# Kernel tuning notes

Hardware: AMD Instinct MI355X
Metric: run time of the kernel (lower is better)

Reference implementation:

```python
import jax, jax.numpy as jnp
import numpy as np

B, P, S, FX, FY, D, DFF = 8, 1, 2048, 16, 16, 512, 2048


def _ln(x, g, b, eps=1e-6):
    m = jnp.mean(x, axis=-1, keepdims=True)
    v = jnp.var(x, axis=-1, keepdims=True)
    return g * (x - m) / jnp.sqrt(v + eps) + b


def setup_inputs() -> dict:
    key = jax.random.key(0)
    ks = jax.random.split(key, 16)
    sc = 0.02
    inp = {
        'inputs': jax.random.normal(ks[0], (B, P, S, FX), dtype=jnp.float32),
        'targets': jax.random.normal(ks[1], (B, P, S, FY), dtype=jnp.float32),
        # input projection Dense(d_model)
        'Wp': jax.random.normal(ks[2], (FX, D), dtype=jnp.float32) * sc,
        'bp': jnp.zeros((D,), jnp.float32),
        # attention projections wq/wk/wv/dense (all Dense(d_model))
        'Wq': jax.random.normal(ks[3], (D, D), dtype=jnp.float32) * sc,
        'bq': jnp.zeros((D,), jnp.float32),
        'Wk': jax.random.normal(ks[4], (D, D), dtype=jnp.float32) * sc,
        'bk': jnp.zeros((D,), jnp.float32),
        'Wv': jax.random.normal(ks[5], (D, D), dtype=jnp.float32) * sc,
        'bv': jnp.zeros((D,), jnp.float32),
        'Wo': jax.random.normal(ks[6], (D, D), dtype=jnp.float32) * sc,
        'bo': jnp.zeros((D,), jnp.float32),
        # layernorm 1 / 2
        'g1': jnp.ones((D,), jnp.float32),
        'beta1': jnp.zeros((D,), jnp.float32),
        'g2': jnp.ones((D,), jnp.float32),
        'beta2': jnp.zeros((D,), jnp.float32),
        # pointwise FFN Dense(dff, relu) -> Dense(d_model)
        'Wf1': jax.random.normal(ks[7], (D, DFF), dtype=jnp.float32) * sc,
        'bf1': jnp.zeros((DFF,), jnp.float32),
        'Wf2': jax.random.normal(ks[8], (DFF, D), dtype=jnp.float32) * sc,
        'bf2': jnp.zeros((D,), jnp.float32),
        # final output layer Dense(output_size)
        'Wfin': jax.random.normal(ks[9], (D, FY), dtype=jnp.float32) * sc,
        'bfin': jnp.zeros((FY,), jnp.float32),
    }
    return inp


def reference(inputs, targets, Wp, bp, Wq, bq, Wk, bk, Wv, bv, Wo, bo,
              g1, beta1, g2, beta2, Wf1, bf1, Wf2, bf2, Wfin, bfin):
    d = jnp.float32(Wp.shape[1])
    # projection_layer_ts then *sqrt(d_model)
    x = (inputs @ Wp + bp) * jnp.sqrt(d)                      # (B,P,S,D)
    q = x @ Wq + bq
    k = x @ Wk + bk
    v = x @ Wv + bv
    # with noise=False and no resampling, the per-step SMC recurrence equals
    # causal self-attention (at step t, K/V hold rows <= t, rest are zero-masked)
    logits = jnp.einsum('bpqd,bpkd->bpqk', q, k) / jnp.sqrt(d)  # (B,P,S,S)
    Sdim = x.shape[2]
    causal = jnp.tril(jnp.ones((Sdim, Sdim), dtype=bool))
    logits = jnp.where(causal, logits, jnp.float32(-1e9))
    attn = jax.nn.softmax(logits, axis=-1)                    # attention weights per step
    z = jnp.einsum('bpqk,bpkd->bpqd', attn, v)
    z = z @ Wo + bo
    # full_model: LN(z+x) -> FFN -> LN(ffn+out)
    out = _ln(z + x, g1, beta1)
    ff = jax.nn.relu(out @ Wf1 + bf1) @ Wf2 + bf2
    r = _ln(ff + out, g2, beta2)                              # R trajectory (B,P,S,D)
    pred = r @ Wfin + bfin                                    # (B,P,S,F_y)
    # no resampling (noise=False): R_resampl == R, pred_resampl == pred
    return (pred, pred, k, v, r, attn)
```

## Files before the change

### kernel.cpp

```cpp
#include <hip/hip_runtime.h>
#include <hip/hip_bf16.h>
#include <stdint.h>

#define BB 8
#define SS 2048
#define TT (BB*SS)
#define DD 512
#define DFFX 2048

static __device__ const float SQRTD  = 22.627416997969522f;
static __device__ const float INVSQD = 0.04419417382415922f;

typedef __attribute__((ext_vector_type(4))) float  f32x4_t;
typedef __attribute__((ext_vector_type(8))) __bf16 bf16x8_t;
typedef __attribute__((ext_vector_type(4))) __bf16 bf16x4_t;

static __device__ __forceinline__ bf16x8_t mk_frag(bf16x4_t lo, bf16x4_t hi) {
  return __builtin_shufflevector(lo, hi, 0, 1, 2, 3, 4, 5, 6, 7);
}

typedef __attribute__((address_space(1))) const unsigned int g_u32;
typedef __attribute__((address_space(3))) unsigned int lds_u32;
static __device__ __forceinline__ void gld16(const void* g, void* l) {
  __builtin_amdgcn_global_load_lds((g_u32*)g, (lds_u32*)l, 16, 0, 0);
}

__global__ __launch_bounds__(256) void transpose_conv_f32(
    const float* __restrict__ src, __bf16* __restrict__ dst, int R, int C) {
  __shared__ float tile[32][33];
  int c0 = blockIdx.x * 32, r0 = blockIdx.y * 32;
  int tx = threadIdx.x & 31, ty = threadIdx.x >> 5;
#pragma unroll
  for (int i = 0; i < 4; i++)
    tile[ty + 8*i][tx] = src[(size_t)(r0 + ty + 8*i) * C + c0 + tx];
  __syncthreads();
#pragma unroll
  for (int i = 0; i < 4; i++)
    dst[(size_t)(c0 + ty + 8*i) * R + r0 + tx] = (__bf16)tile[tx][ty + 8*i];
}

__global__ __launch_bounds__(256) void transpose_bf16(
    const __bf16* __restrict__ src_, __bf16* __restrict__ dst_, int R, int C) {
  __shared__ __bf16 tile[32][34];
  const __bf16* src = src_ + (size_t)blockIdx.z * R * C;
  __bf16* dst = dst_ + (size_t)blockIdx.z * R * C;
  int c0 = blockIdx.x * 32, r0 = blockIdx.y * 32;
  int tx = threadIdx.x & 31, ty = threadIdx.x >> 5;
#pragma unroll
  for (int i = 0; i < 4; i++)
    tile[ty + 8*i][tx] = src[(size_t)(r0 + ty + 8*i) * C + c0 + tx];
  __syncthreads();
#pragma unroll
  for (int i = 0; i < 4; i++)
    dst[(size_t)(c0 + ty + 8*i) * R + r0 + tx] = tile[tx][ty + 8*i];
}

__global__ __launch_bounds__(256) void projx_kernel(
    const float* __restrict__ inp, const float* __restrict__ Wp,
    const float* __restrict__ bp, __bf16* __restrict__ xb) {
  __shared__ float wps[16][512];
  for (int i = threadIdx.x; i < 16 * 512; i += 256) wps[i >> 9][i & 511] = Wp[i];
  __syncthreads();
  const int t = blockIdx.x * 4 + (threadIdx.x >> 6);
  const int li = threadIdx.x & 63;
  float iv[16];
#pragma unroll
  for (int r = 0; r < 16; r++) iv[r] = inp[(size_t)t * 16 + r];
  float acc[8];
#pragma unroll
  for (int j = 0; j < 8; j++) acc[j] = 0.f;
#pragma unroll
  for (int r = 0; r < 16; r++) {
#pragma unroll
    for (int j = 0; j < 8; j++) acc[j] += iv[r] * wps[r][li + 64 * j];
  }
#pragma unroll
  for (int j = 0; j < 8; j++) {
    int c = li + 64 * j;
    xb[(size_t)t * DD + c] = (__bf16)((acc[j] + bp[c]) * SQRTD);
  }
}

template <bool CTRI, bool CAUSAL, bool RELU, bool RES, bool SCALE, bool QKV3>
__global__ __launch_bounds__(256) void gemm128(
    const __bf16* __restrict__ A, const __bf16* __restrict__ Bt,
    const float* __restrict__ bias, const float* __restrict__ bias2,
    const float* __restrict__ bias3, const __bf16* __restrict__ Res,
    __bf16* __restrict__ Cb, float* __restrict__ Cf,
    __bf16* __restrict__ Cb2, float* __restrict__ Cf2,
    __bf16* __restrict__ Cb3, float* __restrict__ Cf3,
    int N, int K, size_t aBatch, size_t bBatch, size_t cBatch) {
  const int n0 = blockIdx.x * 128, m0 = blockIdx.y * 128;
  if (CTRI && n0 > m0 + 127) return;
  __shared__ __align__(16) __bf16 As[3 * 128 * 32];
  __shared__ __align__(16) __bf16 Bs[3 * 128 * 32];
  const int tid = threadIdx.x, lane = tid & 63, wave = tid >> 6;
  const int l15 = lane & 15, g = lane >> 4;
  const int wr = wave >> 1, wc = wave & 1;

  const int srow0 = wave * 32 + (lane >> 2);
  const int srow1 = srow0 + 16;
  const int sc0 = (((lane & 3) ^ ((srow0 >> 1) & 3)) << 4);
  const int sc1 = (((lane & 3) ^ ((srow1 >> 1) & 3)) << 4);
  const size_t aOff = (size_t)blockIdx.z * aBatch;
  const size_t bOff = (size_t)blockIdx.z * bBatch;
  const size_t cOff = (size_t)blockIdx.z * cBatch;
  const char* ga0 = (const char*)(A + aOff + (size_t)(m0 + srow0) * K) + sc0;
  const char* ga1 = (const char*)(A + aOff + (size_t)(m0 + srow1) * K) + sc1;
  const char* gb0 = (const char*)(Bt + bOff + (size_t)(n0 + srow0) * K) + sc0;
  const char* gb1 = (const char*)(Bt + bOff + (size_t)(n0 + srow1) * K) + sc1;

  const int plo = (g >> 1) ^ ((l15 >> 1) & 3);
  const int aof0 = (wr * 64 + l15) * 64 + plo * 16 + (g & 1) * 8;
  const int bof0 = (wc * 64 + l15) * 64 + plo * 16 + (g & 1) * 8;

  f32x4_t acc[4][4];
#pragma unroll
  for (int i = 0; i < 4; i++)
#pragma unroll
    for (int j = 0; j < 4; j++) acc[i][j] = (f32x4_t){0.f, 0.f, 0.f, 0.f};

  auto STAGE = [&](const int buf, const int k0) {
    const size_t kb = (size_t)k0 * 2;
    char* la = (char*)As + buf * 8192 + wave * 2048;
    char* lb = (char*)Bs + buf * 8192 + wave * 2048;
    gld16(ga0 + kb, la);
    gld16(ga1 + kb, la + 1024);
    gld16(gb0 + kb, lb);
    gld16(gb1 + kb, lb + 1024);
  };
  auto COMPUTE = [&](const int buf) {
    const char* AsB = (const char*)As + buf * 8192;
    const char* BsB = (const char*)Bs + buf * 8192;
    bf16x8_t af[4], bfr[4];
#pragma unroll
    for (int i = 0; i < 4; i++) {
      const int ao = aof0 + i * 1024;
      af[i] = mk_frag(*(const bf16x4_t*)(AsB + ao),
                      *(const bf16x4_t*)(AsB + (ao ^ 32)));
      const int bo = bof0 + i * 1024;
      bfr[i] = mk_frag(*(const bf16x4_t*)(BsB + bo),
                       *(const bf16x4_t*)(BsB + (bo ^ 32)));
    }
#pragma unroll
    for (int i = 0; i < 4; i++)
#pragma unroll
      for (int j = 0; j < 4; j++)
        acc[i][j] = __builtin_amdgcn_mfma_f32_16x16x32_bf16(af[i], bfr[j], acc[i][j], 0, 0, 0);
  };

  const int kend = CAUSAL ? (m0 + 128) : K;
  const int nt = kend >> 5;
  STAGE(0, 0);
  STAGE(1, 32);
  STAGE(2, 64);
  int cur = 0;
  for (int t = 0; t < nt; ++t) {
    const int rem = nt - 1 - t;
    if (rem >= 2)      asm volatile("s_waitcnt vmcnt(8)" ::: "memory");
    else if (rem == 1) asm volatile("s_waitcnt vmcnt(4)" ::: "memory");
    else               asm volatile("s_waitcnt vmcnt(0)" ::: "memory");
    __builtin_amdgcn_s_barrier();
    COMPUTE(cur);
    __builtin_amdgcn_s_barrier();
    if (t + 3 < nt) STAGE(cur, (t + 3) << 5);
    cur = (cur == 2) ? 0 : cur + 1;
  }

#pragma unroll
  for (int i = 0; i < 4; i++) {
#pragma unroll
    for (int j = 0; j < 4; j++) {
      const int col = n0 + wc * 64 + j * 16 + l15;
      if (QKV3) {
        const int sub = col >> 9, c5 = col & 511;
        const float bv = (sub == 0 ? bias : sub == 1 ? bias2 : bias3)[c5];
        __bf16* cb = sub == 0 ? Cb : sub == 1 ? Cb2 : Cb3;
        float* cf = sub == 0 ? (float*)nullptr : sub == 1 ? Cf2 : Cf3;
#pragma unroll
        for (int r = 0; r < 4; r++) {
          const int row = m0 + wr * 64 + i * 16 + g * 4 + r;
          const float v = acc[i][j][r] + bv;
          cb[(size_t)row * DD + c5] = (__bf16)v;
          if (cf) cf[(size_t)row * DD + c5] = v;
        }
      } else {
        const float bv = bias ? bias[col] : 0.f;
#pragma unroll
        for (int r = 0; r < 4; r++) {
          const int row = m0 + wr * 64 + i * 16 + g * 4 + r;
          float v = acc[i][j][r];
          if (SCALE) v *= INVSQD;
          v += bv;
          if (RELU) v = fmaxf(v, 0.f);
          if (RES) v += (float)Res[(size_t)row * N + col];
          const size_t cidx = cOff + (size_t)row * N + col;
          if (Cb) Cb[cidx] = (__bf16)v;
          if (Cf) Cf[cidx] = v;
        }
      }
    }
  }
}

__global__ __launch_bounds__(256) void softmax_kernel(
    float* __restrict__ att, __bf16* __restrict__ pb) {
  const int t = blockIdx.x * 4 + (threadIdx.x >> 6);
  const int gq = t & (SS - 1);
  const int lane = threadIdx.x & 63;
  float* row = att + (size_t)t * SS;
  __bf16* prow = pb + (size_t)t * SS;
  const int nch = (gq >> 9) + 1;
  float x[32];
  float m = -1e30f;
#pragma unroll
  for (int ch = 0; ch < 4; ch++) {
    float* xp = &x[ch * 8];
    if (ch < nch) {
      const int c0 = ch * 512 + lane * 8;
      float4 v0 = *(const float4*)(row + c0);
      float4 v1 = *(const float4*)(row + c0 + 4);
      xp[0]=v0.x; xp[1]=v0.y; xp[2]=v0.z; xp[3]=v0.w;
      xp[4]=v1.x; xp[5]=v1.y; xp[6]=v1.z; xp[7]=v1.w;
#pragma unroll
      for (int j = 0; j < 8; j++) {
        xp[j] = (c0 + j <= gq) ? xp[j] : -1e30f;
        m = fmaxf(m, xp[j]);
      }
    } else {
#pragma unroll
      for (int j = 0; j < 8; j++) xp[j] = -1e30f;
    }
  }
#pragma unroll
  for (int off = 1; off < 64; off <<= 1) m = fmaxf(m, __shfl_xor(m, off, 64));
  float s = 0.f;
#pragma unroll
  for (int i = 0; i < 32; i++) { x[i] = __expf(x[i] - m); s += x[i]; }
#pragma unroll
  for (int off = 1; off < 64; off <<= 1) s += __shfl_xor(s, off, 64);
  const float inv = 1.f / s;
#pragma unroll
  for (int ch = 0; ch < 4; ch++) {
    const int c0 = ch * 512 + lane * 8;
    float o[8];
    bf16x8_t ov;
#pragma unroll
    for (int j = 0; j < 8; j++) {
      const float pv = x[ch * 8 + j] * inv;
      o[j] = pv;
      ov[j] = (__bf16)pv;
    }
    float4 f0, f1;
    f0.x = o[0]; f0.y = o[1]; f0.z = o[2]; f0.w = o[3];
    f1.x = o[4]; f1.y = o[5]; f1.z = o[6]; f1.w = o[7];
    *(float4*)(row + c0) = f0;
    *(float4*)(row + c0 + 4) = f1;
    *(bf16x8_t*)(prow + c0) = ov;
  }
}

__global__ __launch_bounds__(256) void ln_kernel(
    const __bf16* __restrict__ X, const float* __restrict__ gam,
    const float* __restrict__ bet, __bf16* __restrict__ Ob, float* __restrict__ Of) {
  const int t = blockIdx.x * 4 + (threadIdx.x >> 6);
  const int lane = threadIdx.x & 63;
  const int d0 = lane * 8;
  bf16x8_t xv = *(const bf16x8_t*)(X + (size_t)t * DD + d0);
  float x[8];
#pragma unroll
  for (int j = 0; j < 8; j++) x[j] = (float)xv[j];
  float s = 0.f, sq = 0.f;
#pragma unroll
  for (int j = 0; j < 8; j++) { s += x[j]; sq += x[j] * x[j]; }
#pragma unroll
  for (int off = 1; off < 64; off <<= 1) {
    s += __shfl_xor(s, off, 64);
    sq += __shfl_xor(sq, off, 64);
  }
  const float mean = s * (1.f / 512.f);
  const float var = sq * (1.f / 512.f) - mean * mean;
  const float rstd = rsqrtf(var + 1e-6f);
  float4 g0 = *(const float4*)(gam + d0), g1v = *(const float4*)(gam + d0 + 4);
  float4 b0 = *(const float4*)(bet + d0), b1v = *(const float4*)(bet + d0 + 4);
  float gg[8] = {g0.x, g0.y, g0.z, g0.w, g1v.x, g1v.y, g1v.z, g1v.w};
  float bb2[8] = {b0.x, b0.y, b0.z, b0.w, b1v.x, b1v.y, b1v.z, b1v.w};
  float o[8];
#pragma unroll
  for (int j = 0; j < 8; j++) o[j] = (x[j] - mean) * rstd * gg[j] + bb2[j];
  if (Ob) {
    bf16x8_t ov;
#pragma unroll
    for (int j = 0; j < 8; j++) ov[j] = (__bf16)o[j];
    *(bf16x8_t*)(Ob + (size_t)t * DD + d0) = ov;
  }
  if (Of) {
    float4 f0; f0.x = o[0]; f0.y = o[1]; f0.z = o[2]; f0.w = o[3];
    float4 f1; f1.x = o[4]; f1.y = o[5]; f1.z = o[6]; f1.w = o[7];
    *(float4*)(Of + (size_t)t * DD + d0) = f0;
    *(float4*)(Of + (size_t)t * DD + d0 + 4) = f1;
  }
}

__global__ __launch_bounds__(256) void final_kernel(
    const float* __restrict__ Rm, const float* __restrict__ Wfin,
    const float* __restrict__ bfin, float* __restrict__ P1, float* __restrict__ P2) {
  __shared__ float wfs[512][17];
  for (int i = threadIdx.x; i < 512 * 16; i += 256) wfs[i >> 4][i & 15] = Wfin[i];
  __syncthreads();
  const int tl = threadIdx.x >> 4, n = threadIdx.x & 15;
  const int t = blockIdx.x * 16 + tl;
  const float* rp = Rm + (size_t)t * DD;
  float acc = 0.f;
#pragma unroll 4
  for (int k = 0; k < 512; k += 4) {
    float4 rv = *(const float4*)(rp + k);
    acc += rv.x * wfs[k][n] + rv.y * wfs[k + 1][n] + rv.z * wfs[k + 2][n] + rv.w * wfs[k + 3][n];
  }
  const float v = acc + bfin[n];
  P1[(size_t)t * 16 + n] = v;
  P2[(size_t)t * 16 + n] = v;
}

extern "C" void kernel_launch(void* const* d_in, const int* in_sizes, int n_in,
                              void* d_out, int out_size, void* d_ws, size_t ws_size,
                              hipStream_t stream) {
  const float* inp  = (const float*)d_in[0];
  const float* Wp   = (const float*)d_in[2];
  const float* bp   = (const float*)d_in[3];
  const float* Wq   = (const float*)d_in[4];
  const float* bq   = (const float*)d_in[5];
  const float* Wk   = (const float*)d_in[6];
  const float* bk   = (const float*)d_in[7];
  const float* Wv   = (const float*)d_in[8];
  const float* bv   = (const float*)d_in[9];
  const float* Wo   = (const float*)d_in[10];
  const float* bo   = (const float*)d_in[11];
  const float* g1   = (const float*)d_in[12];
  const float* be1  = (const float*)d_in[13];
  const float* g2   = (const float*)d_in[14];
  const float* be2  = (const float*)d_in[15];
  const float* Wf1  = (const float*)d_in[16];
  const float* bf1  = (const float*)d_in[17];
  const float* Wf2  = (const float*)d_in[18];
  const float* bf2  = (const float*)d_in[19];
  const float* Wfin = (const float*)d_in[20];
  const float* bfin = (const float*)d_in[21];
  (void)in_sizes; (void)n_in; (void)out_size; (void)ws_size;

  float* out = (float*)d_out;
  float* o_pred1 = out;
  float* o_pred2 = out + 262144;
  float* o_k     = out + 524288;
  float* o_v     = out + 8912896;
  float* o_r     = out + 17301504;
  float* o_att   = out + 25690112;

  char* base = (char*)d_ws;
  size_t off = 0;
  auto take = [&](size_t n) -> __bf16* {
    __bf16* p = (__bf16*)(base + off);
    off += (n * sizeof(__bf16) + 255) & ~(size_t)255;
    return p;
  };
  __bf16* Wqkv_t = take((size_t)3 * DD * DD);
  __bf16* Wo_t   = take((size_t)DD * DD);
  __bf16* Wf1_t  = take((size_t)DD * DFFX);
  __bf16* Wf2_t  = take((size_t)DD * DFFX);
  __bf16* xb     = take((size_t)TT * DD);
  __bf16* qbuf   = take((size_t)TT * DD);
  __bf16* kbuf   = take((size_t)TT * DD);
  __bf16* vbuf   = take((size_t)TT * DD);
  __bf16* zb     = take((size_t)TT * DD);
  __bf16* h1b    = take((size_t)TT * DD);
  __bf16* lninb  = take((size_t)TT * DD);
  __bf16* ffb    = take((size_t)TT * DFFX);
  __bf16* vt     = take((size_t)TT * DD);
  __bf16* pb     = ffb;

  transpose_conv_f32<<<dim3(16, 16), 256, 0, stream>>>(Wq, Wqkv_t, DD, DD);
  transpose_conv_f32<<<dim3(16, 16), 256, 0, stream>>>(Wk, Wqkv_t + (size_t)DD * DD, DD, DD);
  transpose_conv_f32<<<dim3(16, 16), 256, 0, stream>>>(Wv, Wqkv_t + (size_t)2 * DD * DD, DD, DD);
  transpose_conv_f32<<<dim3(16, 16), 256, 0, stream>>>(Wo, Wo_t, DD, DD);
  transpose_conv_f32<<<dim3(64, 16), 256, 0, stream>>>(Wf1, Wf1_t, DD, DFFX);
  transpose_conv_f32<<<dim3(16, 64), 256, 0, stream>>>(Wf2, Wf2_t, DFFX, DD);

  projx_kernel<<<dim3(TT / 4), 256, 0, stream>>>(inp, Wp, bp, xb);

  gemm128<false, false, false, false, false, true><<<dim3(12, 128, 1), 256, 0, stream>>>(
      xb, Wqkv_t, bq, bk, bv, nullptr,
      qbuf, nullptr, kbuf, o_k, vbuf, o_v, 1536, DD, 0, 0, 0);

  gemm128<true, false, false, false, true, false><<<dim3(16, 16, BB), 256, 0, stream>>>(
      qbuf, kbuf, nullptr, nullptr, nullptr, nullptr,
      nullptr, o_att, nullptr, nullptr, nullptr, nullptr, SS, DD,
      (size_t)SS * DD, (size_t)SS * DD, (size_t)SS * SS);

  transpose_bf16<<<dim3(16, 64, BB), 256, 0, stream>>>(vbuf, vt, SS, DD);

  softmax_kernel<<<dim3(TT / 4), 256, 0, stream>>>(o_att, pb);

  gemm128<false, true, false, false, false, false><<<dim3(4, 16, BB), 256, 0, stream>>>(
      pb, vt, nullptr, nullptr, nullptr, nullptr,
      zb, nullptr, nullptr, nullptr, nullptr, nullptr, DD, SS,
      (size_t)SS * SS, (size_t)DD * SS, (size_t)SS * DD);

  gemm128<false, false, false, true, false, false><<<dim3(4, 128, 1), 256, 0, stream>>>(
      zb, Wo_t, bo, nullptr, nullptr, xb,
      lninb, nullptr, nullptr, nullptr, nullptr, nullptr, DD, DD, 0, 0, 0);
  ln_kernel<<<dim3(TT / 4), 256, 0, stream>>>(lninb, g1, be1, h1b, nullptr);

  gemm128<false, false, true, false, false, false><<<dim3(16, 128, 1), 256, 0, stream>>>(
      h1b, Wf1_t, bf1, nullptr, nullptr, nullptr,
      ffb, nullptr, nullptr, nullptr, nullptr, nullptr, DFFX, DD, 0, 0, 0);
  gemm128<false, false, false, true, false, false><<<dim3(4, 128, 1), 256, 0, stream>>>(
      ffb, Wf2_t, bf2, nullptr, nullptr, h1b,
      lninb, nullptr, nullptr, nullptr, nullptr, nullptr, DD, DFFX, 0, 0, 0);

  ln_kernel<<<dim3(TT / 4), 256, 0, stream>>>(lninb, g2, be2, nullptr, o_r);
  final_kernel<<<dim3(TT / 16), 256, 0, stream>>>(o_r, Wfin, bfin, o_pred1, o_pred2);
}
```

Measured before the change: 508.4 us.

## Fold input projection into QKV weights and reassociate Wo before attention

Precomputes Wp·[Wq|Wk|Wv] (with the sqrt(d) scale and the biases folded in) so that Q, K and V come directly from the 16-wide inputs through a small-K kernel, replacing the 1536-wide QKV GEMM. It also applies Wo to V before the attention-weighted sum, using the identity (P·V)·Wo = P·(V·Wo). The bias and residual add then fuse into the PV GEMM epilogue, removing the separate Wo GEMM over all tokens. The cost is an extra per-batch V·Wo GEMM plus a transpose, and changed rounding, since V·Wo is stored in bf16 and the folded weights are stored in fp32.

```diff
diff --git a/kernel.cpp b/kernel.cpp
--- a/kernel.cpp
+++ b/kernel.cpp
@@ -14,6 +14,7 @@
 typedef __attribute__((ext_vector_type(4))) float  f32x4_t;
 typedef __attribute__((ext_vector_type(8))) __bf16 bf16x8_t;
 typedef __attribute__((ext_vector_type(4))) __bf16 bf16x4_t;
+typedef __attribute__((ext_vector_type(2))) __bf16 bf16x2_t;
 
 static __device__ __forceinline__ bf16x8_t mk_frag(bf16x4_t lo, bf16x4_t hi) {
   return __builtin_shufflevector(lo, hi, 0, 1, 2, 3, 4, 5, 6, 7);
@@ -55,40 +56,101 @@
     dst[(size_t)(c0 + ty + 8*i) * R + r0 + tx] = tile[tx][ty + 8*i];
 }
 
-__global__ __launch_bounds__(256) void projx_kernel(
-    const float* __restrict__ inp, const float* __restrict__ Wp,
-    const float* __restrict__ bp, __bf16* __restrict__ xb) {
-  __shared__ float wps[16][512];
-  for (int i = threadIdx.x; i < 16 * 512; i += 256) wps[i >> 9][i & 511] = Wp[i];
+__global__ __launch_bounds__(256) void fold_kernel(
+    const float* __restrict__ Wp, const float* __restrict__ bp,
+    const float* __restrict__ Wq, const float* __restrict__ bq,
+    const float* __restrict__ Wk, const float* __restrict__ bk,
+    const float* __restrict__ Wv, const float* __restrict__ bv,
+    float* __restrict__ Wfold, float* __restrict__ bfold) {
+  __shared__ float wp[16][512];
+  __shared__ float bps[512];
+  for (int i = threadIdx.x; i < 16 * 512; i += 256) wp[i >> 9][i & 511] = Wp[i];
+  for (int i = threadIdx.x; i < 512; i += 256) bps[i] = bp[i];
   __syncthreads();
-  const int t = blockIdx.x * 4 + (threadIdx.x >> 6);
-  const int li = threadIdx.x & 63;
-  float iv[16];
-#pragma unroll
-  for (int r = 0; r < 16; r++) iv[r] = inp[(size_t)t * 16 + r];
-  float acc[8];
-#pragma unroll
-  for (int j = 0; j < 8; j++) acc[j] = 0.f;
+  const int cl = threadIdx.x & 15, r = threadIdx.x >> 4;
+  const int cg = blockIdx.x * 16 + cl;
+  const int sub = cg >> 9, wc = cg & 511;
+  const float* W = sub == 0 ? Wq : sub == 1 ? Wk : Wv;
+  const float* bb = sub == 0 ? bq : sub == 1 ? bk : bv;
+  float acc = 0.f, bacc = 0.f;
+  for (int k = 0; k < 512; k += 4) {
+    const float4 wpv = *(const float4*)&wp[r][k];
+    const float g0 = W[(size_t)k * 512 + wc];
+    const float g1 = W[(size_t)(k + 1) * 512 + wc];
+    const float g2 = W[(size_t)(k + 2) * 512 + wc];
+    const float g3 = W[(size_t)(k + 3) * 512 + wc];
+    acc += wpv.x * g0 + wpv.y * g1 + wpv.z * g2 + wpv.w * g3;
+    if (r == 0) {
+      const float4 b4 = *(const float4*)&bps[k];
+      bacc += b4.x * g0 + b4.y * g1 + b4.z * g2 + b4.w * g3;
+    }
+  }
+  Wfold[(size_t)r * 1536 + cg] = acc * SQRTD;
+  if (r == 0) bfold[cg] = bacc * SQRTD + bb[wc];
+}
+
+__global__ __launch_bounds__(256) void smallk_kernel(
+    const float* __restrict__ inp, const float* __restrict__ Wb, const int ldw,
+    const float* __restrict__ biasb, const float scale,
+    __bf16* __restrict__ ob0, __bf16* __restrict__ ob1, __bf16* __restrict__ ob2,
+    float* __restrict__ fo1, float* __restrict__ fo2) {
+  const int sl = blockIdx.y;
+  const float* W = Wb + sl * 512;
+  const float* bias = biasb + sl * 512;
+  __bf16* ob = sl == 0 ? ob0 : sl == 1 ? ob1 : ob2;
+  float* fo = sl == 0 ? (float*)nullptr : sl == 1 ? fo1 : fo2;
+  __shared__ float ivl[16][16];
+  const int tid = threadIdx.x;
+  ivl[tid >> 4][tid & 15] = inp[(size_t)blockIdx.x * 256 + tid];
+  const int c0 = 2 * tid;
+  float w0[16], w1[16];
 #pragma unroll
   for (int r = 0; r < 16; r++) {
-#pragma unroll
-    for (int j = 0; j < 8; j++) acc[j] += iv[r] * wps[r][li + 64 * j];
-  }
-#pragma unroll
-  for (int j = 0; j < 8; j++) {
-    int c = li + 64 * j;
-    xb[(size_t)t * DD + c] = (__bf16)((acc[j] + bp[c]) * SQRTD);
-  }
-}
-
-template <bool CTRI, bool CAUSAL, bool RELU, bool RES, bool SCALE, bool QKV3>
+    w0[r] = W[(size_t)r * ldw + c0];
+    w1[r] = W[(size_t)r * ldw + c0 + 1];
+  }
+  const float bb0 = bias[c0], bb1 = bias[c0 + 1];
+  __syncthreads();
+#pragma unroll 4
+  for (int tt = 0; tt < 16; ++tt) {
+    const float4 i0 = *(const float4*)&ivl[tt][0];
+    const float4 i1 = *(const float4*)&ivl[tt][4];
+    const float4 i2 = *(const float4*)&ivl[tt][8];
+    const float4 i3 = *(const float4*)&ivl[tt][12];
+    float a0, a1;
+    a0  = i0.x * w0[0];   a1  = i0.x * w1[0];
+    a0 += i0.y * w0[1];   a1 += i0.y * w1[1];
+    a0 += i0.z * w0[2];   a1 += i0.z * w1[2];
+    a0 += i0.w * w0[3];   a1 += i0.w * w1[3];
+    a0 += i1.x * w0[4];   a1 += i1.x * w1[4];
+    a0 += i1.y * w0[5];   a1 += i1.y * w1[5];
+    a0 += i1.z * w0[6];   a1 += i1.z * w1[6];
+    a0 += i1.w * w0[7];   a1 += i1.w * w1[7];
+    a0 += i2.x * w0[8];   a1 += i2.x * w1[8];
+    a0 += i2.y * w0[9];   a1 += i2.y * w1[9];
+    a0 += i2.z * w0[10];  a1 += i2.z * w1[10];
+    a0 += i2.w * w0[11];  a1 += i2.w * w1[11];
+    a0 += i3.x * w0[12];  a1 += i3.x * w1[12];
+    a0 += i3.y * w0[13];  a1 += i3.y * w1[13];
+    a0 += i3.z * w0[14];  a1 += i3.z * w1[14];
+    a0 += i3.w * w0[15];  a1 += i3.w * w1[15];
+    const float v0 = (a0 + bb0) * scale;
+    const float v1 = (a1 + bb1) * scale;
+    const size_t t = (size_t)blockIdx.x * 16 + tt;
+    bf16x2_t pv; pv[0] = (__bf16)v0; pv[1] = (__bf16)v1;
+    *(bf16x2_t*)(ob + t * 512 + c0) = pv;
+    if (fo) {
+      float2 fv; fv.x = v0; fv.y = v1;
+      *(float2*)(fo + t * 512 + c0) = fv;
+    }
+  }
+}
+
+template <bool CTRI, bool CAUSAL, bool RELU, bool RES, bool SCALE>
 __global__ __launch_bounds__(256) void gemm128(
     const __bf16* __restrict__ A, const __bf16* __restrict__ Bt,
-    const float* __restrict__ bias, const float* __restrict__ bias2,
-    const float* __restrict__ bias3, const __bf16* __restrict__ Res,
+    const float* __restrict__ bias, const __bf16* __restrict__ Res,
     __bf16* __restrict__ Cb, float* __restrict__ Cf,
-    __bf16* __restrict__ Cb2, float* __restrict__ Cf2,
-    __bf16* __restrict__ Cb3, float* __restrict__ Cf3,
     int N, int K, size_t aBatch, size_t bBatch, size_t cBatch) {
   const int n0 = blockIdx.x * 128, m0 = blockIdx.y * 128;
   if (CTRI && n0 > m0 + 127) return;
@@ -172,32 +234,18 @@
 #pragma unroll
     for (int j = 0; j < 4; j++) {
       const int col = n0 + wc * 64 + j * 16 + l15;
-      if (QKV3) {
-        const int sub = col >> 9, c5 = col & 511;
-        const float bv = (sub == 0 ? bias : sub == 1 ? bias2 : bias3)[c5];
-        __bf16* cb = sub == 0 ? Cb : sub == 1 ? Cb2 : Cb3;
-        float* cf = sub == 0 ? (float*)nullptr : sub == 1 ? Cf2 : Cf3;
-#pragma unroll
-        for (int r = 0; r < 4; r++) {
-          const int row = m0 + wr * 64 + i * 16 + g * 4 + r;
-          const float v = acc[i][j][r] + bv;
-          cb[(size_t)row * DD + c5] = (__bf16)v;
-          if (cf) cf[(size_t)row * DD + c5] = v;
-        }
-      } else {
-        const float bv = bias ? bias[col] : 0.f;
-#pragma unroll
-        for (int r = 0; r < 4; r++) {
-          const int row = m0 + wr * 64 + i * 16 + g * 4 + r;
-          float v = acc[i][j][r];
-          if (SCALE) v *= INVSQD;
-          v += bv;
-          if (RELU) v = fmaxf(v, 0.f);
-          if (RES) v += (float)Res[(size_t)row * N + col];
-          const size_t cidx = cOff + (size_t)row * N + col;
-          if (Cb) Cb[cidx] = (__bf16)v;
-          if (Cf) Cf[cidx] = v;
-        }
+      const float bv = bias ? bias[col] : 0.f;
+#pragma unroll
+      for (int r = 0; r < 4; r++) {
+        const int row = m0 + wr * 64 + i * 16 + g * 4 + r;
+        float v = acc[i][j][r];
+        if (SCALE) v *= INVSQD;
+        v += bv;
+        if (RELU) v = fmaxf(v, 0.f);
+        if (RES) v += (float)Res[cOff + (size_t)row * N + col];
+        const size_t cidx = cOff + (size_t)row * N + col;
+        if (Cb) Cb[cidx] = (__bf16)v;
+        if (Cf) Cf[cidx] = v;
       }
     }
   }
@@ -358,64 +406,62 @@
 
   char* base = (char*)d_ws;
   size_t off = 0;
-  auto take = [&](size_t n) -> __bf16* {
-    __bf16* p = (__bf16*)(base + off);
-    off += (n * sizeof(__bf16) + 255) & ~(size_t)255;
+  auto takeB = [&](size_t bytes) -> char* {
+    char* p = base + off;
+    off += (bytes + 255) & ~(size_t)255;
     return p;
   };
-  __bf16* Wqkv_t = take((size_t)3 * DD * DD);
-  __bf16* Wo_t   = take((size_t)DD * DD);
-  __bf16* Wf1_t  = take((size_t)DD * DFFX);
-  __bf16* Wf2_t  = take((size_t)DD * DFFX);
-  __bf16* xb     = take((size_t)TT * DD);
-  __bf16* qbuf   = take((size_t)TT * DD);
-  __bf16* kbuf   = take((size_t)TT * DD);
-  __bf16* vbuf   = take((size_t)TT * DD);
-  __bf16* zb     = take((size_t)TT * DD);
-  __bf16* h1b    = take((size_t)TT * DD);
-  __bf16* lninb  = take((size_t)TT * DD);
-  __bf16* ffb    = take((size_t)TT * DFFX);
-  __bf16* vt     = take((size_t)TT * DD);
-  __bf16* pb     = ffb;
-
-  transpose_conv_f32<<<dim3(16, 16), 256, 0, stream>>>(Wq, Wqkv_t, DD, DD);
-  transpose_conv_f32<<<dim3(16, 16), 256, 0, stream>>>(Wk, Wqkv_t + (size_t)DD * DD, DD, DD);
-  transpose_conv_f32<<<dim3(16, 16), 256, 0, stream>>>(Wv, Wqkv_t + (size_t)2 * DD * DD, DD, DD);
+  float*  Wfold = (float*)takeB((size_t)16 * 1536 * 4);
+  float*  bfold = (float*)takeB((size_t)1536 * 4);
+  __bf16* Wo_t  = (__bf16*)takeB((size_t)DD * DD * 2);
+  __bf16* Wf1_t = (__bf16*)takeB((size_t)DD * DFFX * 2);
+  __bf16* Wf2_t = (__bf16*)takeB((size_t)DD * DFFX * 2);
+  __bf16* xb    = (__bf16*)takeB((size_t)TT * DD * 2);
+  __bf16* qbuf  = (__bf16*)takeB((size_t)TT * DD * 2);
+  __bf16* kbuf  = (__bf16*)takeB((size_t)TT * DD * 2);
+  __bf16* vbuf  = (__bf16*)takeB((size_t)TT * DD * 2);
+  __bf16* vwo   = (__bf16*)takeB((size_t)TT * DD * 2);
+  __bf16* vwt   = (__bf16*)takeB((size_t)TT * DD * 2);
+  __bf16* h1b   = (__bf16*)takeB((size_t)TT * DD * 2);
+  __bf16* lninb = (__bf16*)takeB((size_t)TT * DD * 2);
+  __bf16* ffb   = (__bf16*)takeB((size_t)TT * DFFX * 2);
+  __bf16* pb    = ffb;
+
   transpose_conv_f32<<<dim3(16, 16), 256, 0, stream>>>(Wo, Wo_t, DD, DD);
   transpose_conv_f32<<<dim3(64, 16), 256, 0, stream>>>(Wf1, Wf1_t, DD, DFFX);
   transpose_conv_f32<<<dim3(16, 64), 256, 0, stream>>>(Wf2, Wf2_t, DFFX, DD);
 
-  projx_kernel<<<dim3(TT / 4), 256, 0, stream>>>(inp, Wp, bp, xb);
-
-  gemm128<false, false, false, false, false, true><<<dim3(12, 128, 1), 256, 0, stream>>>(
-      xb, Wqkv_t, bq, bk, bv, nullptr,
-      qbuf, nullptr, kbuf, o_k, vbuf, o_v, 1536, DD, 0, 0, 0);
-
-  gemm128<true, false, false, false, true, false><<<dim3(16, 16, BB), 256, 0, stream>>>(
-      qbuf, kbuf, nullptr, nullptr, nullptr, nullptr,
-      nullptr, o_att, nullptr, nullptr, nullptr, nullptr, SS, DD,
+  fold_kernel<<<dim3(96), 256, 0, stream>>>(Wp, bp, Wq, bq, Wk, bk, Wv, bv,
+                                            Wfold, bfold);
+
+  smallk_kernel<<<dim3(TT / 16, 1), 256, 0, stream>>>(
+      inp, Wp, DD, bp, SQRTD, xb, nullptr, nullptr, nullptr, nullptr);
+
+  smallk_kernel<<<dim3(TT / 16, 3), 256, 0, stream>>>(
+      inp, Wfold, 1536, bfold, 1.0f, qbuf, kbuf, vbuf, o_k, o_v);
+
+  gemm128<true, false, false, false, true><<<dim3(16, 16, BB), 256, 0, stream>>>(
+      qbuf, kbuf, nullptr, nullptr, nullptr, o_att, SS, DD,
       (size_t)SS * DD, (size_t)SS * DD, (size_t)SS * SS);
 
-  transpose_bf16<<<dim3(16, 64, BB), 256, 0, stream>>>(vbuf, vt, SS, DD);
+  gemm128<false, false, false, false, false><<<dim3(4, 16, BB), 256, 0, stream>>>(
+      vbuf, Wo_t, nullptr, nullptr, vwo, nullptr, DD, DD,
+      (size_t)SS * DD, 0, (size_t)SS * DD);
+
+  transpose_bf16<<<dim3(16, 64, BB), 256, 0, stream>>>(vwo, vwt, SS, DD);
 
   softmax_kernel<<<dim3(TT / 4), 256, 0, stream>>>(o_att, pb);
 
-  gemm128<false, true, false, false, false, false><<<dim3(4, 16, BB), 256, 0, stream>>>(
-      pb, vt, nullptr, nullptr, nullptr, nullptr,
-      zb, nullptr, nullptr, nullptr, nullptr, nullptr, DD, SS,
+  gemm128<false, true, false, true, false><<<dim3(4, 16, BB), 256, 0, stream>>>(
+      pb, vwt, bo, xb, lninb, nullptr, DD, SS,
       (size_t)SS * SS, (size_t)DD * SS, (size_t)SS * DD);
 
-  gemm128<false, false, false, true, false, false><<<dim3(4, 128, 1), 256, 0, stream>>>(
-      zb, Wo_t, bo, nullptr, nullptr, xb,
-      lninb, nullptr, nullptr, nullptr, nullptr, nullptr, DD, DD, 0, 0, 0);
   ln_kernel<<<dim3(TT / 4), 256, 0, stream>>>(lninb, g1, be1, h1b, nullptr);
 
-  gemm128<false, false, true, false, false, false><<<dim3(16, 128, 1), 256, 0, stream>>>(
-      h1b, Wf1_t, bf1, nullptr, nullptr, nullptr,
-      ffb, nullptr, nullptr, nullptr, nullptr, nullptr, DFFX, DD, 0, 0, 0);
-  gemm128<false, false, false, true, false, false><<<dim3(4, 128, 1), 256, 0, stream>>>(
-      ffb, Wf2_t, bf2, nullptr, nullptr, h1b,
-      lninb, nullptr, nullptr, nullptr, nullptr, nullptr, DD, DFFX, 0, 0, 0);
+  gemm128<false, false, true, false, false><<<dim3(16, 128, 1), 256, 0, stream>>>(
+      h1b, Wf1_t, bf1, nullptr, ffb, nullptr, DFFX, DD, 0, 0, 0);
+  gemm128<false, false, false, true, false><<<dim3(4, 128, 1), 256, 0, stream>>>(
+      ffb, Wf2_t, bf2, h1b, lninb, nullptr, DD, DFFX, 0, 0, 0);
 
   ln_kernel<<<dim3(TT / 4), 256, 0, stream>>>(lninb, g2, be2, nullptr, o_r);
   final_kernel<<<dim3(TT / 16), 256, 0, stream>>>(o_r, Wfin, bfin, o_pred1, o_pred2);
```

New measurement: 510.5 us. Within noise of the previous version (+0.4%).
